# Performance work log

Measured on AMD Instinct MI355X. Metric: run time of the kernel, lower is better.

Reference implementation:

```python
import jax, jax.numpy as jnp
import numpy as np

N_FFT = 200; HOP = 100; N_FREQ = N_FFT // 2 + 1  # 101
EMB = 256; HEADS = 8; DHEAD = EMB // HEADS; DEPTH = 4
N_CH = 23; B = 256; TS = 2000
MASK_RATIO = 0.9


def _layernorm(x, s, b):
    mu = jnp.mean(x, -1, keepdims=True)
    var = jnp.mean((x - mu) ** 2, -1, keepdims=True)
    return (x - mu) * jax.lax.rsqrt(var + 1e-5) * s + b


def _posenc(T, d):
    pos = jnp.arange(T, dtype=jnp.float32)[:, None]
    div = jnp.exp(jnp.arange(0, d, 2, dtype=jnp.float32) * (-np.log(10000.0) / d))
    pe = jnp.zeros((T, d), jnp.float32)
    pe = pe.at[:, 0::2].set(jnp.sin(pos * div))
    pe = pe.at[:, 1::2].set(jnp.cos(pos * div))
    return pe


def setup_inputs() -> dict:
    key = jax.random.key(0)
    ks = jax.random.split(key, 12)
    def n(k, shape):
        return (jax.random.normal(k, shape) * 0.02).astype(jnp.float32)
    T = 1 + (TS - N_FFT) // HOP  # 19
    S = N_CH * T                 # 437
    return dict(
        x=jax.random.normal(ks[0], (B, N_CH, TS), jnp.float32),
        mask_noise=jax.random.uniform(ks[1], (B, S, EMB), dtype=jnp.float32),
        W_proj=n(ks[2], (N_FREQ, EMB)), b_proj=jnp.zeros((EMB,), jnp.float32),
        channel_tokens=n(ks[3], (N_CH, EMB)),
        ln1_s=jnp.ones((DEPTH, EMB), jnp.float32), ln1_b=jnp.zeros((DEPTH, EMB), jnp.float32),
        Wq=n(ks[4], (DEPTH, EMB, EMB)), Wk=n(ks[5], (DEPTH, EMB, EMB)),
        Wv=n(ks[6], (DEPTH, EMB, EMB)), Wo=n(ks[7], (DEPTH, EMB, EMB)),
        bo=jnp.zeros((DEPTH, EMB), jnp.float32),
        ln2_s=jnp.ones((DEPTH, EMB), jnp.float32), ln2_b=jnp.zeros((DEPTH, EMB), jnp.float32),
        W1=n(ks[8], (DEPTH, EMB, 4 * EMB)), b1=jnp.zeros((DEPTH, 4 * EMB), jnp.float32),
        W2=n(ks[9], (DEPTH, 4 * EMB, EMB)), b2=jnp.zeros((DEPTH, EMB), jnp.float32),
    )


def _forward(x, mask_noise, W_proj, b_proj, channel_tokens,
             ln1_s, ln1_b, Wq, Wk, Wv, Wo, bo, ln2_s, ln2_b, W1, b1, W2, b2):
    Bb, C, ts = x.shape
    T = 1 + (ts - N_FFT) // HOP
    # ---- vectorized per-channel STFT (rect window, center=False, onesided) ----
    idx = jnp.arange(T)[:, None] * HOP + jnp.arange(N_FFT)[None, :]  # [T, n_fft]
    frames = x[:, :, idx]                                            # [B,C,T,n_fft]
    spec = jnp.abs(jnp.fft.rfft(frames, axis=-1)).astype(x.dtype)    # [B,C,T,F]
    # patch embedding (Linear over freq), channel token, positional encoding
    emb = spec @ W_proj + b_proj                                     # [B,C,T,E]
    emb = emb + channel_tokens[:C][None, :, None, :]
    emb = emb + _posenc(T, emb.shape[-1])[None, None]
    emb = emb.reshape(Bb, C * T, -1)                                 # [B,S,E]
    # ---- random masking (mask_ratio=0.9 as hard-coded in forward) ----
    mask = mask_noise < MASK_RATIO
    masked = jnp.where(mask, jnp.zeros((), emb.dtype), emb)
    # ---- LinearAttentionTransformer (non-causal linear attention, pre-norm) ----
    h = masked
    for l in range(DEPTH):
        y = _layernorm(h, ln1_s[l], ln1_b[l])
        S = y.shape[1]
        q = (y @ Wq[l]).reshape(Bb, S, HEADS, DHEAD).transpose(0, 2, 1, 3)
        k = (y @ Wk[l]).reshape(Bb, S, HEADS, DHEAD).transpose(0, 2, 1, 3)
        v = (y @ Wv[l]).reshape(Bb, S, HEADS, DHEAD).transpose(0, 2, 1, 3)
        q = jax.nn.softmax(q, axis=-1) * (DHEAD ** -0.5)
        k = jax.nn.softmax(k, axis=2)  # softmax over sequence
        ctx = jnp.einsum('bhnd,bhne->bhde', k, v)     # [B,H,d,d] global context
        att = jnp.einsum('bhnd,bhde->bhne', q, ctx)   # [B,H,S,d]
        att = att.transpose(0, 2, 1, 3).reshape(Bb, S, EMB)
        h = h + att @ Wo[l] + bo[l]
        y = _layernorm(h, ln2_s[l], ln2_b[l])
        h = h + jax.nn.gelu(y @ W1[l] + b1[l]) @ W2[l] + b2[l]
    return emb, masked, h, mask


def reference(x, mask_noise, W_proj, b_proj, channel_tokens,
              ln1_s, ln1_b, Wq, Wk, Wv, Wo, bo, ln2_s, ln2_b, W1, b1, W2, b2):
    return _forward(x, mask_noise, W_proj, b_proj, channel_tokens,
                    ln1_s, ln1_b, Wq, Wk, Wv, Wo, bo, ln2_s, ln2_b, W1, b1, W2, b2)
```

## Files before the change

### kernel.cpp

```cpp
#include <hip/hip_runtime.h>

#define BB    256
#define NCH   23
#define TT    19
#define SS    437
#define BSR   111872
#define EMBD  256
#define NHEAD 8
#define DH    32
#define NFREQ 101
#define NFFT  200
#define HOPSZ 100
#define TSLEN 2000
#define HID   1024
#define NDEPTH 4
#define NTOK  28639232
#define QKVW  768
#define WL    786432

typedef __attribute__((ext_vector_type(8))) __bf16 bf16x8;
typedef __attribute__((ext_vector_type(4))) float  f32x4;

__device__ __forceinline__ float gelu_f(float x){
    return 0.5f*x*(1.0f + tanhf(0.7978845608028654f*(x + 0.044715f*x*x*x)));
}
__device__ __forceinline__ unsigned short f2b(float f){
    unsigned u = __float_as_uint(f);
    return (unsigned short)((u + 0x7FFFu + ((u >> 16) & 1u)) >> 16);
}
__device__ __forceinline__ float b2f(unsigned short h){
    return __uint_as_float(((unsigned)h) << 16);
}

__device__ __forceinline__ void swz_tile(int& bx, int& by){
    int nx = gridDim.x, nwg = nx * gridDim.y;
    int lid = blockIdx.y * nx + blockIdx.x;
    int q = nwg >> 3, r = nwg & 7;
    int xcd = lid & 7, off = lid >> 3;
    int wgid = (xcd < r ? xcd*(q+1) : r*(q+1) + (xcd-r)*q) + off;
    bx = wgid % nx; by = wgid / nx;
}

__global__ void init_twb(unsigned short* __restrict__ tw){
    int i = blockIdx.x*256 + threadIdx.x;
    if(i >= 256*256) return;
    int n = i >> 8, k = i & 255;
    float v = 0.f;
    if(k < NFFT && n < 2*NFREQ){
        int f = n >> 1;
        int ph = (f * k) % NFFT;
        float ang = 6.283185307179586f * (float)ph / (float)NFFT;
        v = (n & 1) ? sinf(ang) : cosf(ang);
    }
    tw[i] = f2b(v);
}

__global__ void init_pe(float* __restrict__ pe){
    int i = blockIdx.x*256 + threadIdx.x;
    if(i >= TT*EMBD) return;
    int t = i / EMBD, e = i % EMBD;
    int j = e >> 1;
    float div = expf((float)(2*j) * (-9.210340371976184f/256.0f));
    float ang = (float)t * div;
    pe[i] = (e & 1) ? cosf(ang) : sinf(ang);
}

__global__ void wprep_proj(const float* __restrict__ Wp, unsigned short* __restrict__ Wt){
    int i = blockIdx.x*256 + threadIdx.x;
    if(i >= 256*128) return;
    int e = i >> 7, k = i & 127;
    Wt[i] = f2b(k < NFREQ ? Wp[(size_t)k*EMBD + e] : 0.f);
}

__global__ void wprep_qkv(const float* __restrict__ Wq, const float* __restrict__ Wk,
                          const float* __restrict__ Wv, unsigned short* __restrict__ wbuf){
    long i = (long)blockIdx.x*256 + threadIdx.x;
    if(i >= (long)NDEPTH*QKVW*EMBD) return;
    int l = (int)(i / (QKVW*EMBD));
    int rem = (int)(i % (QKVW*EMBD));
    int n = rem >> 8, k = rem & 255;
    const float* W = (n < 256) ? Wq : (n < 512) ? Wk : Wv;
    wbuf[(size_t)l*WL + rem] = f2b(W[(size_t)l*65536 + (size_t)k*256 + (n & 255)]);
}
__global__ void wprep_wo(const float* __restrict__ Wo, unsigned short* __restrict__ wbuf){
    int i = blockIdx.x*256 + threadIdx.x;
    if(i >= NDEPTH*65536) return;
    int l = i >> 16, rem = i & 65535;
    int n = rem >> 8, k = rem & 255;
    wbuf[(size_t)l*WL + 196608 + rem] = f2b(Wo[(size_t)l*65536 + (size_t)k*256 + n]);
}
__global__ void wprep_w1(const float* __restrict__ W1, unsigned short* __restrict__ wbuf){
    long i = (long)blockIdx.x*256 + threadIdx.x;
    if(i >= (long)NDEPTH*262144) return;
    int l = (int)(i >> 18), rem = (int)(i & 262143);
    int n = rem >> 8, k = rem & 255;
    wbuf[(size_t)l*WL + 262144 + rem] = f2b(W1[(size_t)l*262144 + (size_t)k*1024 + n]);
}
__global__ void wprep_w2(const float* __restrict__ W2, unsigned short* __restrict__ wbuf){
    long i = (long)blockIdx.x*256 + threadIdx.x;
    if(i >= (long)NDEPTH*262144) return;
    int l = (int)(i >> 18), rem = (int)(i & 262143);
    int n = rem >> 10, k = rem & 1023;
    wbuf[(size_t)l*WL + 524288 + rem] = f2b(W2[(size_t)l*262144 + (size_t)k*256 + n]);
}

__global__ void frames_bf16(const float* __restrict__ x, unsigned short* __restrict__ fr){
    for(long i = (long)blockIdx.x*blockDim.x + threadIdx.x; i < (long)BSR*256;
        i += (long)gridDim.x*blockDim.x){
        int  k   = (int)(i & 255);
        long row = i >> 8;
        int  t   = (int)(row % TT);
        long bc  = row / TT;
        float v = (k < NFFT) ? x[bc*(long)TSLEN + (long)t*HOPSZ + k] : 0.f;
        fr[i] = f2b(v);
    }
}

#define GEMM_CORE(A_, B_, K_) \
    f32x4 acc[4][4]; \
    _Pragma("unroll") \
    for(int i=0;i<4;++i) \
        _Pragma("unroll") \
        for(int jj=0;jj<4;++jj) acc[i][jj] = (f32x4){0.f,0.f,0.f,0.f}; \
    const int srow0 = w*32 + (l>>3); \
    const int sgrp  = l & 7; \
    for(int k0 = 0; k0 < (K_); k0 += 64){ \
        _Pragma("unroll") \
        for(int it=0; it<4; ++it){ \
            int row  = srow0 + it*8; \
            int colA = ((sgrp ^ (row & 7)) << 3); \
            const unsigned short* ga = (A_) + (size_t)(m0+row)*(K_) + k0 + colA; \
            const unsigned short* gb = (B_) + (size_t)(n0+row)*(K_) + k0 + colA; \
            __builtin_amdgcn_global_load_lds( \
                (__attribute__((address_space(1))) void*)ga, \
                (__attribute__((address_space(3))) void*)(As + w*2048 + it*512), \
                16, 0, 0); \
            __builtin_amdgcn_global_load_lds( \
                (__attribute__((address_space(1))) void*)gb, \
                (__attribute__((address_space(3))) void*)(Bs + w*2048 + it*512), \
                16, 0, 0); \
        } \
        __syncthreads(); \
        _Pragma("unroll") \
        for(int kk=0; kk<2; ++kk){ \
            bf16x8 af[4], bfr[4]; \
            _Pragma("unroll") \
            for(int mi=0;mi<4;++mi){ \
                int row = wr*64 + mi*16 + (l & 15); \
                int grp = kk*4 + (l >> 4); \
                af[mi] = *(const bf16x8*)&As[row*64 + ((grp ^ (row&7))<<3)]; \
            } \
            _Pragma("unroll") \
            for(int ni=0;ni<4;++ni){ \
                int row = wc*64 + ni*16 + (l & 15); \
                int grp = kk*4 + (l >> 4); \
                bfr[ni] = *(const bf16x8*)&Bs[row*64 + ((grp ^ (row&7))<<3)]; \
            } \
            _Pragma("unroll") \
            for(int mi=0;mi<4;++mi) \
                _Pragma("unroll") \
                for(int ni=0;ni<4;++ni) \
                    acc[mi][ni] = __builtin_amdgcn_mfma_f32_16x16x32_bf16( \
                        af[mi], bfr[ni], acc[mi][ni], 0, 0, 0); \
        } \
        __syncthreads(); \
    }

template<int MODE>
__global__ __launch_bounds__(256) void gemm_mfma(
    const unsigned short* __restrict__ A, const unsigned short* __restrict__ Bt,
    const float* __restrict__ bias, void* __restrict__ Cv,
    const unsigned short* __restrict__ Cin, int M, int N, int K)
{
    __shared__ __align__(16) unsigned short As[128*64];
    __shared__ __align__(16) unsigned short Bs[128*64];
    const int tid = threadIdx.x;
    const int w = tid >> 6, l = tid & 63;
    int bx, by; swz_tile(bx, by);
    const int m0 = by * 128, n0 = bx * 128;
    const int wr = w >> 1, wc = w & 1;
    GEMM_CORE(A, Bt, K)
    const int cn  = l & 15;
    const int cr4 = (l >> 4) * 4;
    #pragma unroll
    for(int ni=0;ni<4;++ni){
        int n = n0 + wc*64 + ni*16 + cn;
        float bn = (MODE==1 || MODE==2 || MODE==4) ? bias[n] : 0.f;
        #pragma unroll
        for(int mi=0;mi<4;++mi){
            int mB = m0 + wr*64 + mi*16 + cr4;
            #pragma unroll
            for(int r=0;r<4;++r){
                size_t off = (size_t)(mB+r)*N + n;
                float v = acc[mi][ni][r];
                if(MODE == 1){
                    ((unsigned short*)Cv)[off] = f2b(b2f(Cin[off]) + v + bn);
                } else if(MODE == 2){
                    ((unsigned short*)Cv)[off] = f2b(gelu_f(v + bn));
                } else if(MODE == 3){
                    ((unsigned short*)Cv)[off] = f2b(v);
                } else {
                    ((float*)Cv)[off] = b2f(Cin[off]) + v + bn;
                }
            }
        }
    }
}

__global__ __launch_bounds__(256) void gemm_dft(
    const unsigned short* __restrict__ A, const unsigned short* __restrict__ Bt,
    unsigned short* __restrict__ spec)
{
    const int K = 256;
    __shared__ __align__(16) unsigned short As[128*64];
    __shared__ __align__(16) unsigned short Bs[128*64];
    const int tid = threadIdx.x;
    const int w = tid >> 6, l = tid & 63;
    int bx, by; swz_tile(bx, by);
    const int m0 = by * 128, n0 = bx * 128;
    const int wr = w >> 1, wc = w & 1;
    GEMM_CORE(A, Bt, K)
    const int cn  = l & 15;
    const int cr4 = (l >> 4) * 4;
    #pragma unroll
    for(int ni=0;ni<4;++ni){
        int n = n0 + wc*64 + ni*16 + cn;
        #pragma unroll
        for(int mi=0;mi<4;++mi){
            int mB = m0 + wr*64 + mi*16 + cr4;
            #pragma unroll
            for(int r=0;r<4;++r){
                float own = acc[mi][ni][r];
                float par = __shfl_xor(own, 1, 64);
                if(!(cn & 1)){
                    float sv = sqrtf(own*own + par*par);
                    spec[(size_t)(mB+r)*128 + (n >> 1)] = f2b(sv);
                }
            }
        }
    }
}

__global__ __launch_bounds__(256) void gemm_emb(
    const unsigned short* __restrict__ A, const unsigned short* __restrict__ Bt,
    const float* __restrict__ bp, const float* __restrict__ ctok,
    const float* __restrict__ pe, const float* __restrict__ noise,
    float* __restrict__ o_emb, float* __restrict__ o_masked,
    float* __restrict__ o_mask, unsigned short* __restrict__ bufH)
{
    const int K = 128, N = 256;
    __shared__ __align__(16) unsigned short As[128*64];
    __shared__ __align__(16) unsigned short Bs[128*64];
    const int tid = threadIdx.x;
    const int w = tid >> 6, l = tid & 63;
    int bx, by; swz_tile(bx, by);
    const int m0 = by * 128, n0 = bx * 128;
    const int wr = w >> 1, wc = w & 1;
    GEMM_CORE(A, Bt, K)
    const int cn  = l & 15;
    const int cr4 = (l >> 4) * 4;
    #pragma unroll
    for(int ni=0;ni<4;++ni){
        int n = n0 + wc*64 + ni*16 + cn;
        float bn = bp[n];
        #pragma unroll
        for(int mi=0;mi<4;++mi){
            int mB = m0 + wr*64 + mi*16 + cr4;
            #pragma unroll
            for(int r=0;r<4;++r){
                int m = mB + r;
                int t = m % TT;
                int c = (m / TT) % NCH;
                size_t off = (size_t)m*EMBD + n;
                float v = acc[mi][ni][r] + bn + ctok[c*EMBD + n] + pe[t*EMBD + n];
                o_emb[off] = v;
                float mn = noise[off];
                bool  msk = mn < 0.9f;
                float md = msk ? 0.f : v;
                bufH[off]     = f2b(md);
                o_masked[off] = md;
                o_mask[off]   = msk ? 1.f : 0.f;
            }
        }
    }
}

__global__ __launch_bounds__(256) void ln_bf16(const unsigned short* __restrict__ X,
    const float* __restrict__ s, const float* __restrict__ b,
    unsigned short* __restrict__ Y)
{
    int w = threadIdx.x >> 6, lane = threadIdx.x & 63;
    long row = (long)blockIdx.x*4 + w;
    ushort4 u = *(const ushort4*)(X + row*EMBD + lane*4);
    float x0 = b2f(u.x), x1 = b2f(u.y), x2 = b2f(u.z), x3 = b2f(u.w);
    float sum = x0 + x1 + x2 + x3;
    #pragma unroll
    for(int o=32;o>0;o>>=1) sum += __shfl_xor(sum, o, 64);
    float mu = sum * (1.0f/256.0f);
    float dx = x0-mu, dy = x1-mu, dz = x2-mu, dw = x3-mu;
    float vs = dx*dx + dy*dy + dz*dz + dw*dw;
    #pragma unroll
    for(int o=32;o>0;o>>=1) vs += __shfl_xor(vs, o, 64);
    float rstd = rsqrtf(vs*(1.0f/256.0f) + 1e-5f);
    float4 s4 = *(const float4*)(s + lane*4);
    float4 b4 = *(const float4*)(b + lane*4);
    ushort4 o4;
    o4.x = f2b(dx*rstd*s4.x + b4.x);
    o4.y = f2b(dy*rstd*s4.y + b4.y);
    o4.z = f2b(dz*rstd*s4.z + b4.z);
    o4.w = f2b(dw*rstd*s4.w + b4.w);
    *(ushort4*)(Y + row*EMBD + lane*4) = o4;
}

__global__ __launch_bounds__(256) void ctx_kernel(const unsigned short* __restrict__ qkvb,
    float* __restrict__ ctx)
{
    __shared__ float kt[16][DH], vt[16][DH];
    __shared__ float sm[8][32], ss[8][32];
    __shared__ float kmsL[32], kinvL[32];
    int bh = blockIdx.x; int b = bh >> 3, h = bh & 7;
    int tid = threadIdx.x;

    {
        int d = tid & 31, g = tid >> 5;
        const unsigned short* p = qkvb + (size_t)b*SS*QKVW + 256 + h*DH + d;
        float m = -1e30f, s = 0.f;
        for(int n = g; n < SS; n += 8){
            float xv = b2f(p[(size_t)n*QKVW]);
            if(xv > m){ s = s*expf(m-xv) + 1.f; m = xv; }
            else      { s += expf(xv-m); }
        }
        sm[g][d] = m; ss[g][d] = s;
    }
    __syncthreads();
    if(tid < 32){
        float M = sm[0][tid], S = ss[0][tid];
        #pragma unroll
        for(int o = 1; o < 8; ++o){
            float m2 = sm[o][tid], s2 = ss[o][tid];
            if(m2 > M){ S = S*expf(M-m2) + s2; M = m2; }
            else      { S += s2*expf(m2-M); }
        }
        kmsL[tid] = M; kinvL[tid] = 1.0f / S;
    }
    __syncthreads();

    int d = tid >> 3, e4 = (tid & 7) * 4;
    float km = kmsL[d];
    float a0=0,a1=0,a2=0,a3=0;
    for(int n0=0;n0<SS;n0+=16){
        __syncthreads();
        #pragma unroll
        for(int i=0;i<2;++i){
            int e = tid + i*256;
            int nn = e >> 5, dd = e & 31;
            int n = n0 + nn;
            float kv, vv;
            if(n < SS){
                size_t off = ((size_t)(b*SS+n))*QKVW + h*DH + dd;
                kv = b2f(qkvb[off + 256]);
                vv = b2f(qkvb[off + 512]);
            } else { kv = -1e30f; vv = 0.f; }
            kt[nn][dd] = kv; vt[nn][dd] = vv;
        }
        __syncthreads();
        #pragma unroll
        for(int nn=0;nn<16;++nn){
            float ke = expf(kt[nn][d] - km);
            a0 = fmaf(ke, vt[nn][e4+0], a0);
            a1 = fmaf(ke, vt[nn][e4+1], a1);
            a2 = fmaf(ke, vt[nn][e4+2], a2);
            a3 = fmaf(ke, vt[nn][e4+3], a3);
        }
    }
    float inv = kinvL[d];
    float* op = ctx + ((size_t)bh*DH + d)*DH + e4;
    op[0]=a0*inv; op[1]=a1*inv; op[2]=a2*inv; op[3]=a3*inv;
}

__global__ __launch_bounds__(256) void att_kernel(const unsigned short* __restrict__ qkvb,
    const float* __restrict__ ctx, unsigned short* __restrict__ att)
{
    __shared__ float qs[4][EMBD];
    int w = threadIdx.x >> 6, lane = threadIdx.x & 63;
    int b = blockIdx.y;
    int s = blockIdx.x*4 + w;
    if(s >= SS) return;
    long row = (long)b*SS + s;
    ushort4 qu = *(const ushort4*)(qkvb + (size_t)row*QKVW + lane*4);
    float4 q4 = make_float4(b2f(qu.x), b2f(qu.y), b2f(qu.z), b2f(qu.w));
    float m = fmaxf(fmaxf(q4.x,q4.y), fmaxf(q4.z,q4.w));
    #pragma unroll
    for(int o=1;o<8;o<<=1) m = fmaxf(m, __shfl_xor(m, o, 64));
    float e0 = expf(q4.x-m), e1 = expf(q4.y-m), e2 = expf(q4.z-m), e3 = expf(q4.w-m);
    float ssum = e0+e1+e2+e3;
    #pragma unroll
    for(int o=1;o<8;o<<=1) ssum += __shfl_xor(ssum, o, 64);
    float sc = 0.17677669529663687f / ssum;
    *(float4*)&qs[w][lane*4] = make_float4(e0*sc, e1*sc, e2*sc, e3*sc);
    int head = lane >> 3;
    int ecol = (lane & 7) * 4;
    const float* cb = ctx + ((size_t)(b*NHEAD + head))*DH*DH + ecol;
    float a0=0,a1=0,a2=0,a3=0;
    #pragma unroll
    for(int d=0; d<DH; ++d){
        float qd = qs[w][head*DH + d];
        float4 c4 = *(const float4*)(cb + d*DH);
        a0 = fmaf(qd, c4.x, a0);
        a1 = fmaf(qd, c4.y, a1);
        a2 = fmaf(qd, c4.z, a2);
        a3 = fmaf(qd, c4.w, a3);
    }
    ushort4 o4; o4.x=f2b(a0); o4.y=f2b(a1); o4.z=f2b(a2); o4.w=f2b(a3);
    *(ushort4*)(att + row*EMBD + lane*4) = o4;
}

extern "C" void kernel_launch(void* const* d_in, const int* in_sizes, int n_in,
                              void* d_out, int out_size, void* d_ws, size_t ws_size,
                              hipStream_t stream)
{
    if(n_in != 18) return;

    const float* x     = (const float*)d_in[0];
    const float* noise = (const float*)d_in[1];
    const float* Wproj = (const float*)d_in[2];
    const float* bproj = (const float*)d_in[3];
    const float* ctok  = (const float*)d_in[4];
    const float* ln1s  = (const float*)d_in[5];
    const float* ln1b  = (const float*)d_in[6];
    const float* Wq    = (const float*)d_in[7];
    const float* Wk    = (const float*)d_in[8];
    const float* Wv    = (const float*)d_in[9];
    const float* Wo    = (const float*)d_in[10];
    const float* bo    = (const float*)d_in[11];
    const float* ln2s  = (const float*)d_in[12];
    const float* ln2b  = (const float*)d_in[13];
    const float* W1    = (const float*)d_in[14];
    const float* b1    = (const float*)d_in[15];
    const float* W2    = (const float*)d_in[16];
    const float* b2    = (const float*)d_in[17];

    char* p = (char*)d_ws;
    unsigned short* bufHb = (unsigned short*)p;           p += (size_t)NTOK*2;
    float* big = (float*)p;                               p += (size_t)NTOK*2*4;
    unsigned short* qkvb   = (unsigned short*)big;
    unsigned short* hidb   = (unsigned short*)big;
    unsigned short* specb  = (unsigned short*)p;          p += (size_t)BSR*128*2;
    unsigned short* bufYb  = (unsigned short*)p;          p += (size_t)NTOK*2;
    unsigned short* framesb= bufYb;
    unsigned short* attb   = bufYb;
    float* ctxb = (float*)p;                              p += (size_t)BB*NHEAD*DH*DH*4;
    float* peb  = (float*)p;                              p += (size_t)TT*EMBD*4;
    unsigned short* twb  = (unsigned short*)p;            p += (size_t)65536*2;
    unsigned short* Wpb  = (unsigned short*)p;            p += (size_t)32768*2;
    unsigned short* wbuf = (unsigned short*)p;            p += (size_t)4*WL*2;
    if(ws_size < (size_t)(p - (char*)d_ws)) return;

    float* out      = (float*)d_out;
    float* o_emb    = out;
    float* o_masked = out + (size_t)NTOK;
    float* o_h      = out + 2*(size_t)NTOK;
    float* o_mask   = out + 3*(size_t)NTOK;

    dim3 blk(256);

    init_twb<<<256, blk, 0, stream>>>(twb);
    init_pe <<<19,  blk, 0, stream>>>(peb);
    wprep_proj<<<128, blk, 0, stream>>>(Wproj, Wpb);
    wprep_qkv<<<3072, blk, 0, stream>>>(Wq, Wk, Wv, wbuf);
    wprep_wo <<<1024, blk, 0, stream>>>(Wo, wbuf);
    wprep_w1 <<<4096, blk, 0, stream>>>(W1, wbuf);
    wprep_w2 <<<4096, blk, 0, stream>>>(W2, wbuf);

    frames_bf16<<<4096, blk, 0, stream>>>(x, framesb);
    gemm_dft<<<dim3(2,874), blk, 0, stream>>>(framesb, twb, specb);
    gemm_emb<<<dim3(2,874), blk, 0, stream>>>(specb, Wpb, bproj, ctok, peb, noise,
                                              o_emb, o_masked, o_mask, bufHb);

    for(int l=0;l<NDEPTH;++l){
        unsigned short* wl   = wbuf + (size_t)l*WL;
        unsigned short* Wqkv = wl;
        unsigned short* Wot  = wl + 196608;
        unsigned short* W1t  = wl + 262144;
        unsigned short* W2t  = wl + 524288;

        ln_bf16<<<BSR/4, blk, 0, stream>>>(bufHb, ln1s + l*EMBD, ln1b + l*EMBD, bufYb);
        gemm_mfma<3><<<dim3(6,874), blk, 0, stream>>>(bufYb, Wqkv, nullptr, qkvb,
                                                      nullptr, BSR, QKVW, EMBD);
        ctx_kernel<<<BB*NHEAD, blk, 0, stream>>>(qkvb, ctxb);
        att_kernel<<<dim3(110, BB), blk, 0, stream>>>(qkvb, ctxb, attb);
        gemm_mfma<1><<<dim3(2,874), blk, 0, stream>>>(attb, Wot, bo + l*EMBD, bufHb,
                                                      bufHb, BSR, EMBD, EMBD);
        ln_bf16<<<BSR/4, blk, 0, stream>>>(bufHb, ln2s + l*EMBD, ln2b + l*EMBD, bufYb);
        gemm_mfma<2><<<dim3(8,874), blk, 0, stream>>>(bufYb, W1t, b1 + l*HID, hidb,
                                                      nullptr, BSR, HID, EMBD);
        if(l == NDEPTH-1)
            gemm_mfma<4><<<dim3(2,874), blk, 0, stream>>>(hidb, W2t, b2 + l*EMBD, o_h,
                                                          bufHb, BSR, EMBD, HID);
        else
            gemm_mfma<1><<<dim3(2,874), blk, 0, stream>>>(hidb, W2t, b2 + l*EMBD, bufHb,
                                                          bufHb, BSR, EMBD, HID);
    }
}
```

Before: 3.305 ms.

## Fold LayerNorm into QKV/FFN GEMM epilogues and fuse framing into DFT GEMM

LayerNorm is moved into the following GEMM. The scale is folded into the bf16 weights, and per-column sums of scale*W and bias*W are precomputed. A light row_stats kernel writes per-row mean and rstd, and the GEMM epilogue applies y = rstd*(acc - mu*c) + d. This removes the normalized bf16 activation buffer write and read. Separately, the frames_bf16 kernel is removed by having the DFT GEMM read x directly, convert it to bf16 and store it into LDS. The costs are lower precision, since the mean subtraction now happens after the bf16 matmul (a cancellation risk), and uncoalesced scalar loads in the DFT A-tile.

```diff
diff --git a/kernel.cpp b/kernel.cpp
--- a/kernel.cpp
+++ b/kernel.cpp
@@ -17,8 +17,10 @@
 #define NTOK  28639232
 #define QKVW  768
 #define WL    786432
+#define CDL   3584
 
 typedef __attribute__((ext_vector_type(8))) __bf16 bf16x8;
+typedef __attribute__((ext_vector_type(8))) unsigned short u16x8;
 typedef __attribute__((ext_vector_type(4))) float  f32x4;
 
 __device__ __forceinline__ float gelu_f(float x){
@@ -73,14 +75,16 @@
 }
 
 __global__ void wprep_qkv(const float* __restrict__ Wq, const float* __restrict__ Wk,
-                          const float* __restrict__ Wv, unsigned short* __restrict__ wbuf){
+                          const float* __restrict__ Wv, const float* __restrict__ ln1s,
+                          unsigned short* __restrict__ wbuf){
     long i = (long)blockIdx.x*256 + threadIdx.x;
     if(i >= (long)NDEPTH*QKVW*EMBD) return;
     int l = (int)(i / (QKVW*EMBD));
     int rem = (int)(i % (QKVW*EMBD));
     int n = rem >> 8, k = rem & 255;
     const float* W = (n < 256) ? Wq : (n < 512) ? Wk : Wv;
-    wbuf[(size_t)l*WL + rem] = f2b(W[(size_t)l*65536 + (size_t)k*256 + (n & 255)]);
+    float s = ln1s[l*EMBD + k];
+    wbuf[(size_t)l*WL + rem] = f2b(s * W[(size_t)l*65536 + (size_t)k*256 + (n & 255)]);
 }
 __global__ void wprep_wo(const float* __restrict__ Wo, unsigned short* __restrict__ wbuf){
     int i = blockIdx.x*256 + threadIdx.x;
@@ -89,12 +93,14 @@
     int n = rem >> 8, k = rem & 255;
     wbuf[(size_t)l*WL + 196608 + rem] = f2b(Wo[(size_t)l*65536 + (size_t)k*256 + n]);
 }
-__global__ void wprep_w1(const float* __restrict__ W1, unsigned short* __restrict__ wbuf){
+__global__ void wprep_w1(const float* __restrict__ W1, const float* __restrict__ ln2s,
+                         unsigned short* __restrict__ wbuf){
     long i = (long)blockIdx.x*256 + threadIdx.x;
     if(i >= (long)NDEPTH*262144) return;
     int l = (int)(i >> 18), rem = (int)(i & 262143);
     int n = rem >> 8, k = rem & 255;
-    wbuf[(size_t)l*WL + 262144 + rem] = f2b(W1[(size_t)l*262144 + (size_t)k*1024 + n]);
+    float s = ln2s[l*EMBD + k];
+    wbuf[(size_t)l*WL + 262144 + rem] = f2b(s * W1[(size_t)l*262144 + (size_t)k*1024 + n]);
 }
 __global__ void wprep_w2(const float* __restrict__ W2, unsigned short* __restrict__ wbuf){
     long i = (long)blockIdx.x*256 + threadIdx.x;
@@ -104,15 +110,34 @@
     wbuf[(size_t)l*WL + 524288 + rem] = f2b(W2[(size_t)l*262144 + (size_t)k*256 + n]);
 }
 
-__global__ void frames_bf16(const float* __restrict__ x, unsigned short* __restrict__ fr){
-    for(long i = (long)blockIdx.x*blockDim.x + threadIdx.x; i < (long)BSR*256;
-        i += (long)gridDim.x*blockDim.x){
-        int  k   = (int)(i & 255);
-        long row = i >> 8;
-        int  t   = (int)(row % TT);
-        long bc  = row / TT;
-        float v = (k < NFFT) ? x[bc*(long)TSLEN + (long)t*HOPSZ + k] : 0.f;
-        fr[i] = f2b(v);
+__global__ void prep_cd(const float* __restrict__ Wq, const float* __restrict__ Wk,
+                        const float* __restrict__ Wv, const float* __restrict__ W1,
+                        const float* __restrict__ ln1s, const float* __restrict__ ln1b,
+                        const float* __restrict__ ln2s, const float* __restrict__ ln2b,
+                        const float* __restrict__ b1, float* __restrict__ cd){
+    int i = blockIdx.x*256 + threadIdx.x;
+    if(i >= NDEPTH*1792) return;
+    int l = i / 1792, r = i % 1792;
+    float c = 0.f, d = 0.f;
+    if(r < 768){
+        const float* W = (r < 256) ? Wq : (r < 512) ? Wk : Wv;
+        int n = r & 255;
+        for(int k = 0; k < 256; ++k){
+            float w = W[(size_t)l*65536 + (size_t)k*256 + n];
+            c = fmaf(ln1s[l*EMBD+k], w, c);
+            d = fmaf(ln1b[l*EMBD+k], w, d);
+        }
+        cd[(size_t)l*CDL + r]       = c;
+        cd[(size_t)l*CDL + 768 + r] = d;
+    } else {
+        int n = r - 768;
+        for(int k = 0; k < 256; ++k){
+            float w = W1[(size_t)l*262144 + (size_t)k*1024 + n];
+            c = fmaf(ln2s[l*EMBD+k], w, c);
+            d = fmaf(ln2b[l*EMBD+k], w, d);
+        }
+        cd[(size_t)l*CDL + 1536 + n] = c;
+        cd[(size_t)l*CDL + 2560 + n] = d + b1[l*HID + n];
     }
 }
 
@@ -141,6 +166,11 @@
                 16, 0, 0); \
         } \
         __syncthreads(); \
+        GEMM_MFMA_PHASE \
+        __syncthreads(); \
+    }
+
+#define GEMM_MFMA_PHASE \
         _Pragma("unroll") \
         for(int kk=0; kk<2; ++kk){ \
             bf16x8 af[4], bfr[4]; \
@@ -162,15 +192,16 @@
                 for(int ni=0;ni<4;++ni) \
                     acc[mi][ni] = __builtin_amdgcn_mfma_f32_16x16x32_bf16( \
                         af[mi], bfr[ni], acc[mi][ni], 0, 0, 0); \
-        } \
-        __syncthreads(); \
-    }
+        }
 
 template<int MODE>
 __global__ __launch_bounds__(256) void gemm_mfma(
     const unsigned short* __restrict__ A, const unsigned short* __restrict__ Bt,
     const float* __restrict__ bias, void* __restrict__ Cv,
-    const unsigned short* __restrict__ Cin, int M, int N, int K)
+    const unsigned short* __restrict__ Cin,
+    const float* __restrict__ muv, const float* __restrict__ rsv,
+    const float* __restrict__ cvec, const float* __restrict__ dvec,
+    int M, int N, int K)
 {
     __shared__ __align__(16) unsigned short As[128*64];
     __shared__ __align__(16) unsigned short Bs[128*64];
@@ -182,10 +213,23 @@
     GEMM_CORE(A, Bt, K)
     const int cn  = l & 15;
     const int cr4 = (l >> 4) * 4;
+    float muT[4][4], rsT[4][4];
+    if(MODE == 5 || MODE == 6){
+        #pragma unroll
+        for(int mi=0;mi<4;++mi)
+            #pragma unroll
+            for(int r=0;r<4;++r){
+                int m = m0 + wr*64 + mi*16 + cr4 + r;
+                muT[mi][r] = muv[m];
+                rsT[mi][r] = rsv[m];
+            }
+    }
     #pragma unroll
     for(int ni=0;ni<4;++ni){
         int n = n0 + wc*64 + ni*16 + cn;
-        float bn = (MODE==1 || MODE==2 || MODE==4) ? bias[n] : 0.f;
+        float bn = (MODE==1 || MODE==4) ? bias[n] : 0.f;
+        float cv = (MODE==5 || MODE==6) ? cvec[n] : 0.f;
+        float dv = (MODE==5 || MODE==6) ? dvec[n] : 0.f;
         #pragma unroll
         for(int mi=0;mi<4;++mi){
             int mB = m0 + wr*64 + mi*16 + cr4;
@@ -195,12 +239,11 @@
                 float v = acc[mi][ni][r];
                 if(MODE == 1){
                     ((unsigned short*)Cv)[off] = f2b(b2f(Cin[off]) + v + bn);
-                } else if(MODE == 2){
-                    ((unsigned short*)Cv)[off] = f2b(gelu_f(v + bn));
-                } else if(MODE == 3){
-                    ((unsigned short*)Cv)[off] = f2b(v);
+                } else if(MODE == 4){
+                    ((float*)Cv)[off] = b2f(Cin[off]) + v + bn;
                 } else {
-                    ((float*)Cv)[off] = b2f(Cin[off]) + v + bn;
+                    float y = rsT[mi][r]*v - rsT[mi][r]*muT[mi][r]*cv + dv;
+                    ((unsigned short*)Cv)[off] = f2b(MODE==6 ? gelu_f(y) : y);
                 }
             }
         }
@@ -208,7 +251,7 @@
 }
 
 __global__ __launch_bounds__(256) void gemm_dft(
-    const unsigned short* __restrict__ A, const unsigned short* __restrict__ Bt,
+    const float* __restrict__ x, const unsigned short* __restrict__ Bt,
     unsigned short* __restrict__ spec)
 {
     const int K = 256;
@@ -219,7 +262,40 @@
     int bx, by; swz_tile(bx, by);
     const int m0 = by * 128, n0 = bx * 128;
     const int wr = w >> 1, wc = w & 1;
-    GEMM_CORE(A, Bt, K)
+    f32x4 acc[4][4];
+    #pragma unroll
+    for(int i=0;i<4;++i)
+        #pragma unroll
+        for(int jj=0;jj<4;++jj) acc[i][jj] = (f32x4){0.f,0.f,0.f,0.f};
+    const int sgrp = l & 7;
+    for(int k0 = 0; k0 < K; k0 += 64){
+        #pragma unroll
+        for(int it=0; it<4; ++it){
+            int row = w*32 + it*8 + (l>>3);
+            int kg  = sgrp ^ (row & 7);
+            int kb  = k0 + kg*8;
+            int m   = m0 + row;
+            int t   = m % TT;
+            long bc = m / TT;
+            const float* src = x + bc*(long)TSLEN + (long)t*HOPSZ + kb;
+            u16x8 v;
+            #pragma unroll
+            for(int j=0;j<8;++j){
+                float f = (kb + j < NFFT) ? src[j] : 0.f;
+                v[j] = f2b(f);
+            }
+            *(u16x8*)&As[row*64 + sgrp*8] = v;
+            int colB = (kg << 3);
+            const unsigned short* gb = Bt + (size_t)(n0+row)*K + k0 + colB;
+            __builtin_amdgcn_global_load_lds(
+                (__attribute__((address_space(1))) void*)gb,
+                (__attribute__((address_space(3))) void*)(Bs + w*2048 + it*512),
+                16, 0, 0);
+        }
+        __syncthreads();
+        GEMM_MFMA_PHASE
+        __syncthreads();
+    }
     const int cn  = l & 15;
     const int cr4 = (l >> 4) * 4;
     #pragma unroll
@@ -285,9 +361,8 @@
     }
 }
 
-__global__ __launch_bounds__(256) void ln_bf16(const unsigned short* __restrict__ X,
-    const float* __restrict__ s, const float* __restrict__ b,
-    unsigned short* __restrict__ Y)
+__global__ __launch_bounds__(256) void row_stats(const unsigned short* __restrict__ X,
+    float* __restrict__ muv, float* __restrict__ rsv)
 {
     int w = threadIdx.x >> 6, lane = threadIdx.x & 63;
     long row = (long)blockIdx.x*4 + w;
@@ -301,15 +376,10 @@
     float vs = dx*dx + dy*dy + dz*dz + dw*dw;
     #pragma unroll
     for(int o=32;o>0;o>>=1) vs += __shfl_xor(vs, o, 64);
-    float rstd = rsqrtf(vs*(1.0f/256.0f) + 1e-5f);
-    float4 s4 = *(const float4*)(s + lane*4);
-    float4 b4 = *(const float4*)(b + lane*4);
-    ushort4 o4;
-    o4.x = f2b(dx*rstd*s4.x + b4.x);
-    o4.y = f2b(dy*rstd*s4.y + b4.y);
-    o4.z = f2b(dz*rstd*s4.z + b4.z);
-    o4.w = f2b(dw*rstd*s4.w + b4.w);
-    *(ushort4*)(Y + row*EMBD + lane*4) = o4;
+    if(lane == 0){
+        muv[row] = mu;
+        rsv[row] = rsqrtf(vs*(1.0f/256.0f) + 1e-5f);
+    }
 }
 
 __global__ __launch_bounds__(256) void ctx_kernel(const unsigned short* __restrict__ qkvb,
@@ -320,7 +390,6 @@
     __shared__ float kmsL[32], kinvL[32];
     int bh = blockIdx.x; int b = bh >> 3, h = bh & 7;
     int tid = threadIdx.x;
-
     {
         int d = tid & 31, g = tid >> 5;
         const unsigned short* p = qkvb + (size_t)b*SS*QKVW + 256 + h*DH + d;
@@ -344,7 +413,6 @@
         kmsL[tid] = M; kinvL[tid] = 1.0f / S;
     }
     __syncthreads();
-
     int d = tid >> 3, e4 = (tid & 7) * 4;
     float km = kmsL[d];
     float a0=0,a1=0,a2=0,a3=0;
@@ -446,9 +514,10 @@
     unsigned short* qkvb   = (unsigned short*)big;
     unsigned short* hidb   = (unsigned short*)big;
     unsigned short* specb  = (unsigned short*)p;          p += (size_t)BSR*128*2;
-    unsigned short* bufYb  = (unsigned short*)p;          p += (size_t)NTOK*2;
-    unsigned short* framesb= bufYb;
-    unsigned short* attb   = bufYb;
+    unsigned short* attb   = (unsigned short*)p;          p += (size_t)NTOK*2;
+    float* muv  = (float*)p;                              p += (size_t)BSR*4;
+    float* rsv  = (float*)p;                              p += (size_t)BSR*4;
+    float* cdb  = (float*)p;                              p += (size_t)NDEPTH*CDL*4;
     float* ctxb = (float*)p;                              p += (size_t)BB*NHEAD*DH*DH*4;
     float* peb  = (float*)p;                              p += (size_t)TT*EMBD*4;
     unsigned short* twb  = (unsigned short*)p;            p += (size_t)65536*2;
@@ -467,13 +536,13 @@
     init_twb<<<256, blk, 0, stream>>>(twb);
     init_pe <<<19,  blk, 0, stream>>>(peb);
     wprep_proj<<<128, blk, 0, stream>>>(Wproj, Wpb);
-    wprep_qkv<<<3072, blk, 0, stream>>>(Wq, Wk, Wv, wbuf);
+    wprep_qkv<<<3072, blk, 0, stream>>>(Wq, Wk, Wv, ln1s, wbuf);
     wprep_wo <<<1024, blk, 0, stream>>>(Wo, wbuf);
-    wprep_w1 <<<4096, blk, 0, stream>>>(W1, wbuf);
+    wprep_w1 <<<4096, blk, 0, stream>>>(W1, ln2s, wbuf);
     wprep_w2 <<<4096, blk, 0, stream>>>(W2, wbuf);
-
-    frames_bf16<<<4096, blk, 0, stream>>>(x, framesb);
-    gemm_dft<<<dim3(2,874), blk, 0, stream>>>(framesb, twb, specb);
+    prep_cd  <<<28,   blk, 0, stream>>>(Wq, Wk, Wv, W1, ln1s, ln1b, ln2s, ln2b, b1, cdb);
+
+    gemm_dft<<<dim3(2,874), blk, 0, stream>>>(x, twb, specb);
     gemm_emb<<<dim3(2,874), blk, 0, stream>>>(specb, Wpb, bproj, ctok, peb, noise,
                                               o_emb, o_masked, o_mask, bufHb);
 
@@ -483,22 +552,29 @@
         unsigned short* Wot  = wl + 196608;
         unsigned short* W1t  = wl + 262144;
         unsigned short* W2t  = wl + 524288;
-
-        ln_bf16<<<BSR/4, blk, 0, stream>>>(bufHb, ln1s + l*EMBD, ln1b + l*EMBD, bufYb);
-        gemm_mfma<3><<<dim3(6,874), blk, 0, stream>>>(bufYb, Wqkv, nullptr, qkvb,
-                                                      nullptr, BSR, QKVW, EMBD);
+        float* cq = cdb + (size_t)l*CDL;
+        float* dq = cq + 768;
+        float* c1 = cq + 1536;
+        float* d1 = cq + 2560;
+
+        row_stats<<<BSR/4, blk, 0, stream>>>(bufHb, muv, rsv);
+        gemm_mfma<5><<<dim3(6,874), blk, 0, stream>>>(bufHb, Wqkv, nullptr, qkvb,
+                                    nullptr, muv, rsv, cq, dq, BSR, QKVW, EMBD);
         ctx_kernel<<<BB*NHEAD, blk, 0, stream>>>(qkvb, ctxb);
         att_kernel<<<dim3(110, BB), blk, 0, stream>>>(qkvb, ctxb, attb);
         gemm_mfma<1><<<dim3(2,874), blk, 0, stream>>>(attb, Wot, bo + l*EMBD, bufHb,
-                                                      bufHb, BSR, EMBD, EMBD);
-        ln_bf16<<<BSR/4, blk, 0, stream>>>(bufHb, ln2s + l*EMBD, ln2b + l*EMBD, bufYb);
-        gemm_mfma<2><<<dim3(8,874), blk, 0, stream>>>(bufYb, W1t, b1 + l*HID, hidb,
-                                                      nullptr, BSR, HID, EMBD);
+                                    bufHb, nullptr, nullptr, nullptr, nullptr,
+                                    BSR, EMBD, EMBD);
+        row_stats<<<BSR/4, blk, 0, stream>>>(bufHb, muv, rsv);
+        gemm_mfma<6><<<dim3(8,874), blk, 0, stream>>>(bufHb, W1t, nullptr, hidb,
+                                    nullptr, muv, rsv, c1, d1, BSR, HID, EMBD);
         if(l == NDEPTH-1)
             gemm_mfma<4><<<dim3(2,874), blk, 0, stream>>>(hidb, W2t, b2 + l*EMBD, o_h,
-                                                          bufHb, BSR, EMBD, HID);
+                                    bufHb, nullptr, nullptr, nullptr, nullptr,
+                                    BSR, EMBD, HID);
         else
             gemm_mfma<1><<<dim3(2,874), blk, 0, stream>>>(hidb, W2t, b2 + l*EMBD, bufHb,
-                                                          bufHb, BSR, EMBD, HID);
-    }
-}
+                                    bufHb, nullptr, nullptr, nullptr, nullptr,
+                                    BSR, EMBD, HID);
+    }
+}
```

Result: slower. 3.851 ms (+16.5%).
